# Kernel tuning notes

Measured on AMD Instinct MI355X. Metric: run time of the kernel, lower is better.

Reference implementation:

```python
import jax, jax.numpy as jnp
import numpy as np

EPS = 1e-5

def _ln(x, g, b):
    m = jnp.mean(x, axis=-1, keepdims=True)
    v = jnp.var(x, axis=-1, keepdims=True)
    return (x - m) / jnp.sqrt(v + EPS) * g + b

def setup_inputs() -> dict:
    key = jax.random.key(0)
    ks = jax.random.split(key, 16)
    B, N, CZ, C = 1, 512, 128, 16
    s_cz = 1.0 / np.sqrt(CZ)
    s_c = 1.0 / np.sqrt(C)
    def lin(k, fan_in, shape):
        return jax.random.uniform(k, shape, jnp.float32, -1.0, 1.0) / np.sqrt(fan_in)
    return {
        'x': jax.random.normal(ks[0], (B, N, N, CZ), jnp.float32),
        'Wa1': lin(ks[1], CZ, (CZ, C)), 'ba1': lin(ks[2], CZ, (C,)),
        'Wa2': lin(ks[3], CZ, (CZ, C)), 'ba2': lin(ks[4], CZ, (C,)),
        'Wb1': lin(ks[5], CZ, (CZ, C)), 'bb1': lin(ks[6], CZ, (C,)),
        'Wb2': lin(ks[7], CZ, (CZ, C)), 'bb2': lin(ks[8], CZ, (C,)),
        'ln2_g': jnp.ones((C,), jnp.float32), 'ln2_b': jnp.zeros((C,), jnp.float32),
        'Wg': lin(ks[9], CZ, (CZ, CZ)), 'bg': lin(ks[10], CZ, (CZ,)),
        'Wz': lin(ks[11], C, (C, CZ)), 'bz': lin(ks[12], C, (CZ,)),
    }

def reference(x, Wa1, ba1, Wa2, ba2, Wb1, bb1, Wb2, bb2, ln2_g, ln2_b, Wg, bg, Wz, bz):
    # NOTE: original code computes z=ln1(x) then overwrites z=x, so ln1 is a no-op.
    direction = 'outgoing'
    a = jax.nn.sigmoid((x @ Wa1 + ba1) * (x @ Wa2 + ba2))  # [B,N,N,c]
    b = jax.nn.sigmoid((x @ Wb1 + bb1) * (x @ Wb2 + bb2))  # [B,N,N,c]
    if direction == 'incoming':
        a = jnp.swapaxes(a, 1, 2)
        b = jnp.swapaxes(b, 1, 2)
    g = jax.nn.sigmoid(x @ Wg + bg)  # [B,N,N,c_z]
    # z[b,i,j,c] = sum_k a[b,i,k,c] * b[b,k,j,c]  (per-channel triangle matmul)
    z = jnp.einsum('bikc,bkjc->bijc', a, b)
    return g * (_ln(z, ln2_g, ln2_b) @ Wz + bz)
```

## Files before the change

### kernel.cpp

```cpp
#include <hip/hip_runtime.h>


#define NN 512
#define PP (NN*NN)
#define CZD 128
#define CD 16
#define LN_EPS 1e-5f

typedef unsigned short u16;
typedef __bf16 bf16x8 __attribute__((ext_vector_type(8)));
typedef float  f32x4  __attribute__((ext_vector_type(4)));

#define OFF_A  0u
#define OFF_B  8388608u
#define OFF_Z  16777216u
#define OFF_G  33554432u
#define OFF_WT 100663296u
#define OFF_BC 100712448u

__device__ __forceinline__ float bf2f(u16 u) {
    union { unsigned int i; float f; } v; v.i = ((unsigned int)u) << 16; return v.f;
}
__device__ __forceinline__ u16 f2bf(float f) {
    union { __bf16 b; u16 u; } v; v.b = (__bf16)f; return v.u;
}
__device__ __forceinline__ float sigmoidf(float x) { return 1.0f / (1.0f + __expf(-x)); }

__device__ __forceinline__ int swz(int row, int bytecol) {
    return row * 256 + ((((bytecol >> 4) + row) & 15) << 4) + (bytecol & 15);
}

__global__ void pack_w(const float* __restrict__ Wa1, const float* __restrict__ Wa2,
                       const float* __restrict__ Wb1, const float* __restrict__ Wb2,
                       const float* __restrict__ Wg,
                       const float* __restrict__ ba1, const float* __restrict__ ba2,
                       const float* __restrict__ bb1, const float* __restrict__ bb2,
                       const float* __restrict__ bg,
                       u16* __restrict__ wt, float* __restrict__ bc) {
    int idx = blockIdx.x * 256 + threadIdx.x;
    int n = idx >> 7, k = idx & 127;
    float v;
    if      (n < 16) v = Wa1[k * CD + n];
    else if (n < 32) v = Wa2[k * CD + (n - 16)];
    else if (n < 48) v = Wb1[k * CD + (n - 32)];
    else if (n < 64) v = Wb2[k * CD + (n - 48)];
    else             v = Wg [k * CZD + (n - 64)];
    wt[n * CZD + k] = f2bf(v);
    if (idx < 192) {
        float b;
        if      (idx < 16) b = ba1[idx];
        else if (idx < 32) b = ba2[idx - 16];
        else if (idx < 48) b = bb1[idx - 32];
        else if (idx < 64) b = bb2[idx - 48];
        else               b = bg [idx - 64];
        bc[idx] = b;
    }
}

__global__ __launch_bounds__(512, 4) void proj_kernel(const float* __restrict__ x,
                                                      const u16* __restrict__ wt,
                                                      const float* __restrict__ bc,
                                                      u16* __restrict__ a_ws, u16* __restrict__ b_ws,
                                                      u16* __restrict__ g_ws) {
    __shared__ __align__(16) char lds[49152];
    char* Wl = lds;
    char* aT = lds;
    char* bT = lds + 4096;
    char* gT = lds + 8192;
    const int t = threadIdx.x;
    const int wv = t >> 6, lane = t & 63, l16 = lane & 15, quad = lane >> 4;
    const long pos0 = (long)blockIdx.x * 128;

    const float* xrow = x + (pos0 + wv * 16 + l16) * CZD + quad * 8;
    float4 xa[4][2];
#pragma unroll
    for (int ks = 0; ks < 4; ++ks) {
        xa[ks][0] = *reinterpret_cast<const float4*>(xrow + ks * 32);
        xa[ks][1] = *reinterpret_cast<const float4*>(xrow + ks * 32 + 4);
    }

#pragma unroll
    for (int i = 0; i < 6; ++i) {
        int c = t + 512 * i;
        int n = c >> 4, g = c & 15;
        uint4 v = *reinterpret_cast<const uint4*>(wt + n * CZD + g * 8);
        *reinterpret_cast<uint4*>(Wl + swz(n, g * 16)) = v;
    }

    bf16x8 af[4];
#pragma unroll
    for (int ks = 0; ks < 4; ++ks) {
        union { u16 s[8]; bf16x8 v; } tb;
        tb.s[0] = f2bf(xa[ks][0].x); tb.s[1] = f2bf(xa[ks][0].y);
        tb.s[2] = f2bf(xa[ks][0].z); tb.s[3] = f2bf(xa[ks][0].w);
        tb.s[4] = f2bf(xa[ks][1].x); tb.s[5] = f2bf(xa[ks][1].y);
        tb.s[6] = f2bf(xa[ks][1].z); tb.s[7] = f2bf(xa[ks][1].w);
        af[ks] = tb.v;
    }
    __syncthreads();

    f32x4 acc[12];
#pragma unroll
    for (int ct = 0; ct < 12; ++ct) acc[ct] = (f32x4){0.f, 0.f, 0.f, 0.f};
#pragma unroll
    for (int ks = 0; ks < 4; ++ks)
#pragma unroll
        for (int ct = 0; ct < 12; ++ct) {
            bf16x8 wb = *reinterpret_cast<const bf16x8*>(Wl + swz(ct * 16 + l16, ks * 64 + quad * 16));
            acc[ct] = __builtin_amdgcn_mfma_f32_16x16x32_bf16(af[ks], wb, acc[ct], 0, 0, 0);
        }
    __syncthreads();

    {
        const float ba1 = bc[l16], ba2 = bc[16 + l16], bb1 = bc[32 + l16], bb2 = bc[48 + l16];
        u16 av[4], bv[4];
#pragma unroll
        for (int r = 0; r < 4; ++r) {
            av[r] = f2bf(sigmoidf((acc[0][r] + ba1) * (acc[1][r] + ba2)));
            bv[r] = f2bf(sigmoidf((acc[2][r] + bb1) * (acc[3][r] + bb2)));
        }
        *reinterpret_cast<uint2*>(aT + swz(l16, wv * 32 + quad * 8)) = *reinterpret_cast<const uint2*>(av);
        *reinterpret_cast<uint2*>(bT + swz(l16, wv * 32 + quad * 8)) = *reinterpret_cast<const uint2*>(bv);
#pragma unroll
        for (int ct = 0; ct < 8; ++ct) {
            const float bgv = bc[64 + ct * 16 + l16];
#pragma unroll
            for (int r = 0; r < 4; ++r) {
                int pos = wv * 16 + quad * 4 + r;
                *reinterpret_cast<u16*>(gT + swz(pos, ct * 32 + l16 * 2)) =
                    f2bf(sigmoidf(acc[4 + ct][r] + bgv));
            }
        }
    }
    __syncthreads();

    if (t < 256) {
        int ch = t >> 4, i = t & 15;
        uint4 v = *reinterpret_cast<const uint4*>(aT + swz(ch, i * 16));
        *reinterpret_cast<uint4*>(a_ws + (long)ch * PP + pos0 + i * 8) = v;
    } else {
        int u = t - 256;
        int ch = u >> 4, i = u & 15;
        uint4 v = *reinterpret_cast<const uint4*>(bT + swz(ch, i * 16));
        *reinterpret_cast<uint4*>(b_ws + (long)ch * PP + pos0 + i * 8) = v;
    }
#pragma unroll
    for (int i = 0; i < 4; ++i) {
        int c = t + 512 * i;
        int pos = c >> 4, g = c & 15;
        uint4 v = *reinterpret_cast<const uint4*>(gT + swz(pos, g * 16));
        *reinterpret_cast<uint4*>(g_ws + (pos0 + pos) * CZD + g * 8) = v;
    }
}

__global__ __launch_bounds__(512) void tri_kernel(const u16* __restrict__ a_ws,
                                                  const u16* __restrict__ b_ws,
                                                  float* __restrict__ z_ws) {
    __shared__ __align__(16) char Alds[16384];
    __shared__ __align__(16) char Btl [16384];
    __shared__ __align__(16) char Brow[16384];
    const int t = threadIdx.x;
    const int wv = t >> 6, lane = t & 63, l16 = lane & 15, quad = lane >> 4;
    const int wr = wv >> 2, wc = wv & 3;
    const int c = blockIdx.y;
    const int i0 = (blockIdx.x >> 2) * 128, j0 = (blockIdx.x & 3) * 128;
    const u16* Ap = a_ws + (long)c * PP;
    const u16* Bp = b_ws + (long)c * PP;

    f32x4 acc[4][2];
#pragma unroll
    for (int m = 0; m < 4; ++m)
#pragma unroll
        for (int n = 0; n < 2; ++n) acc[m][n] = (f32x4){0.f, 0.f, 0.f, 0.f};

    for (int k0 = 0; k0 < NN; k0 += 64) {
#pragma unroll
        for (int i = 0; i < 2; ++i) {
            int ch = t + 512 * i;
            int r = ch >> 3, ko = (ch & 7) * 8;
            uint4 v = *reinterpret_cast<const uint4*>(Ap + (long)(i0 + r) * NN + k0 + ko);
            *reinterpret_cast<uint4*>(Alds + r * 128 + ((ko * 2) ^ ((r & 7) << 4))) = v;
        }
#pragma unroll
        for (int i = 0; i < 2; ++i) {
            int ch = t + 512 * i;
            int k = ch >> 4, jo = (ch & 15) * 8;
            uint4 v = *reinterpret_cast<const uint4*>(Bp + (long)(k0 + k) * NN + j0 + jo);
            *reinterpret_cast<uint4*>(Brow + k * 256 + jo * 2) = v;
        }
        __syncthreads();
#pragma unroll
        for (int i = 0; i < 2; ++i) {
            int ch = t + 512 * i;
            int j = ch & 127, kg = ch >> 7;
            union { u16 s[8]; uint4 v; } tb;
#pragma unroll
            for (int m = 0; m < 8; ++m)
                tb.s[m] = *reinterpret_cast<const u16*>(Brow + (kg * 8 + m) * 256 + j * 2);
            *reinterpret_cast<uint4*>(Btl + j * 128 + ((kg ^ (j & 7)) << 4)) = tb.v;
        }
        __syncthreads();
#pragma unroll
        for (int ks = 0; ks < 2; ++ks) {
            bf16x8 af[4];
#pragma unroll
            for (int m = 0; m < 4; ++m) {
                int row = wr * 64 + m * 16 + l16;
                af[m] = *reinterpret_cast<const bf16x8*>(
                    Alds + row * 128 + ((ks * 64 + quad * 16) ^ ((row & 7) << 4)));
            }
#pragma unroll
            for (int n = 0; n < 2; ++n) {
                int jrow = wc * 32 + n * 16 + l16;
                bf16x8 bf = *reinterpret_cast<const bf16x8*>(
                    Btl + jrow * 128 + (((ks * 4 + quad) ^ (jrow & 7)) << 4));
#pragma unroll
                for (int m = 0; m < 4; ++m)
                    acc[m][n] = __builtin_amdgcn_mfma_f32_16x16x32_bf16(af[m], bf, acc[m][n], 0, 0, 0);
            }
        }
        __syncthreads();
    }
    float* Zp = z_ws + (long)c * PP;
#pragma unroll
    for (int m = 0; m < 4; ++m)
#pragma unroll
        for (int n = 0; n < 2; ++n)
#pragma unroll
            for (int r = 0; r < 4; ++r)
                Zp[(long)(i0 + wr * 64 + m * 16 + quad * 4 + r) * NN + j0 + wc * 32 + n * 16 + l16]
                    = acc[m][n][r];
}

__global__ __launch_bounds__(512) void out_kernel(const float* __restrict__ z_ws,
                                                  const u16* __restrict__ g_ws,
                                                  const float* __restrict__ Wz, const float* __restrict__ bz,
                                                  const float* __restrict__ lng, const float* __restrict__ lnb,
                                                  float* __restrict__ out) {
    __shared__ __align__(16) float zt[16][128];
    __shared__ __align__(16) float nl[128][20];
    __shared__ __align__(16) float wzs[16][128];
    __shared__ float bzl[128];
    __shared__ float lg[16], lb[16];
    const int t = threadIdx.x;
    const long pos0 = (long)blockIdx.x * 128;

    {
        int ch = t >> 5, off = (t & 31) * 4;
        const float4 v = *reinterpret_cast<const float4*>(z_ws + (long)ch * PP + pos0 + off);
        *reinterpret_cast<float4*>(&zt[ch][off]) = v;
    }
    {
        int idx = t * 4;
        const float4 v = *reinterpret_cast<const float4*>(Wz + idx);
        *reinterpret_cast<float4*>(&wzs[idx >> 7][idx & 127]) = v;
    }
    if (t < 128)      bzl[t] = bz[t];
    else if (t < 144) lg[t - 128] = lng[t - 128];
    else if (t < 160) lb[t - 144] = lnb[t - 144];
    __syncthreads();

    {
        int p = t & 127, cgr = t >> 7;
        float m = 0.f;
#pragma unroll
        for (int c0 = 0; c0 < 16; ++c0) m += zt[c0][p];
        m *= (1.f / 16.f);
        float v = 0.f;
#pragma unroll
        for (int c0 = 0; c0 < 16; ++c0) { float d = zt[c0][p] - m; v += d * d; }
        v *= (1.f / 16.f);
        float s = rsqrtf(v + LN_EPS);
#pragma unroll
        for (int cc = 0; cc < 4; ++cc) {
            int c0 = cgr * 4 + cc;
            nl[p][c0] = (zt[c0][p] - m) * s * lg[c0] + lb[c0];
        }
    }
    __syncthreads();

    const int czp = (t & 63) * 2, pg = t >> 6;
    float wzr[32];
#pragma unroll
    for (int c0 = 0; c0 < 16; ++c0) {
        wzr[2 * c0]     = wzs[c0][czp];
        wzr[2 * c0 + 1] = wzs[c0][czp + 1];
    }
    const float bz0 = bzl[czp], bz1 = bzl[czp + 1];
    const unsigned int* gp = reinterpret_cast<const unsigned int*>(g_ws);
#pragma unroll
    for (int pp2 = 0; pp2 < 16; ++pp2) {
        int p = pg * 16 + pp2;
        const float4* np = reinterpret_cast<const float4*>(&nl[p][0]);
        float y0 = bz0, y1 = bz1;
#pragma unroll
        for (int c4 = 0; c4 < 4; ++c4) {
            float4 nv = np[c4];
            y0 += nv.x * wzr[(c4 * 4 + 0) * 2] + nv.y * wzr[(c4 * 4 + 1) * 2] +
                  nv.z * wzr[(c4 * 4 + 2) * 2] + nv.w * wzr[(c4 * 4 + 3) * 2];
            y1 += nv.x * wzr[(c4 * 4 + 0) * 2 + 1] + nv.y * wzr[(c4 * 4 + 1) * 2 + 1] +
                  nv.z * wzr[(c4 * 4 + 2) * 2 + 1] + nv.w * wzr[(c4 * 4 + 3) * 2 + 1];
        }
        long o = (pos0 + p) * CZD + czp;
        unsigned int gg = gp[o >> 1];
        float g0 = bf2f((u16)(gg & 0xffffu));
        float g1 = bf2f((u16)(gg >> 16));
        float2 res; res.x = g0 * y0; res.y = g1 * y1;
        *reinterpret_cast<float2*>(out + o) = res;
    }
}

extern "C" void kernel_launch(void* const* d_in, const int* in_sizes, int n_in,
                              void* d_out, int out_size, void* d_ws, size_t ws_size,
                              hipStream_t stream) {
    const float* x   = (const float*)d_in[0];
    const float* Wa1 = (const float*)d_in[1];
    const float* ba1 = (const float*)d_in[2];
    const float* Wa2 = (const float*)d_in[3];
    const float* ba2 = (const float*)d_in[4];
    const float* Wb1 = (const float*)d_in[5];
    const float* bb1 = (const float*)d_in[6];
    const float* Wb2 = (const float*)d_in[7];
    const float* bb2 = (const float*)d_in[8];
    const float* lng = (const float*)d_in[9];
    const float* lnb = (const float*)d_in[10];
    const float* Wg  = (const float*)d_in[11];
    const float* bg  = (const float*)d_in[12];
    const float* Wz  = (const float*)d_in[13];
    const float* bz  = (const float*)d_in[14];
    float* out = (float*)d_out;
    char* ws = (char*)d_ws;
    u16*   a_ws = (u16*)(ws + OFF_A);
    u16*   b_ws = (u16*)(ws + OFF_B);
    float* z_ws = (float*)(ws + OFF_Z);
    u16*   g_ws = (u16*)(ws + OFF_G);
    u16*   wt   = (u16*)(ws + OFF_WT);
    float* bc   = (float*)(ws + OFF_BC);

    hipLaunchKernelGGL(pack_w, dim3(96), dim3(256), 0, stream,
                       Wa1, Wa2, Wb1, Wb2, Wg, ba1, ba2, bb1, bb2, bg, wt, bc);
    hipLaunchKernelGGL(proj_kernel, dim3(2048), dim3(512), 0, stream, x, wt, bc, a_ws, b_ws, g_ws);
    hipLaunchKernelGGL(tri_kernel, dim3(16, 16), dim3(512), 0, stream, a_ws, b_ws, z_ws);
    hipLaunchKernelGGL(out_kernel, dim3(2048), dim3(512), 0, stream, z_ws, g_ws, Wz, bz, lng, lnb, out);
}
```

Before: 318.2 us.

## Transpose B directly into LDS and double-tile the output kernel with z prefetch

```diff
diff --git a/kernel.cpp b/kernel.cpp
--- a/kernel.cpp
+++ b/kernel.cpp
@@ -158,7 +158,6 @@
                                                   float* __restrict__ z_ws) {
     __shared__ __align__(16) char Alds[16384];
     __shared__ __align__(16) char Btl [16384];
-    __shared__ __align__(16) char Brow[16384];
     const int t = threadIdx.x;
     const int wv = t >> 6, lane = t & 63, l16 = lane & 15, quad = lane >> 4;
     const int wr = wv >> 2, wc = wv & 3;
@@ -183,21 +182,17 @@
         }
 #pragma unroll
         for (int i = 0; i < 2; ++i) {
-            int ch = t + 512 * i;
-            int k = ch >> 4, jo = (ch & 15) * 8;
-            uint4 v = *reinterpret_cast<const uint4*>(Bp + (long)(k0 + k) * NN + j0 + jo);
-            *reinterpret_cast<uint4*>(Brow + k * 256 + jo * 2) = v;
-        }
-        __syncthreads();
-#pragma unroll
-        for (int i = 0; i < 2; ++i) {
-            int ch = t + 512 * i;
-            int j = ch & 127, kg = ch >> 7;
-            union { u16 s[8]; uint4 v; } tb;
-#pragma unroll
-            for (int m = 0; m < 8; ++m)
-                tb.s[m] = *reinterpret_cast<const u16*>(Brow + (kg * 8 + m) * 256 + j * 2);
-            *reinterpret_cast<uint4*>(Btl + j * 128 + ((kg ^ (j & 7)) << 4)) = tb.v;
+            int chk = t + 512 * i;
+            int k = chk >> 4, jo = (chk & 15) * 8;
+            union { uint4 v; u16 s[8]; } tb;
+            tb.v = *reinterpret_cast<const uint4*>(Bp + (long)(k0 + k) * NN + j0 + jo);
+            const int kg = k >> 3, kl = (k & 7) * 2;
+#pragma unroll
+            for (int jj = 0; jj < 8; ++jj) {
+                int j = jo + jj;
+                int gran = ((kg ^ (j & 7)) + (j >> 3)) & 7;
+                *reinterpret_cast<u16*>(Btl + j * 128 + gran * 16 + kl) = tb.s[jj];
+            }
         }
         __syncthreads();
 #pragma unroll
@@ -212,8 +207,8 @@
 #pragma unroll
             for (int n = 0; n < 2; ++n) {
                 int jrow = wc * 32 + n * 16 + l16;
-                bf16x8 bf = *reinterpret_cast<const bf16x8*>(
-                    Btl + jrow * 128 + (((ks * 4 + quad) ^ (jrow & 7)) << 4));
+                int gran = (((ks * 4 + quad) ^ (jrow & 7)) + (jrow >> 3)) & 7;
+                bf16x8 bf = *reinterpret_cast<const bf16x8*>(Btl + jrow * 128 + gran * 16);
 #pragma unroll
                 for (int m = 0; m < 4; ++m)
                     acc[m][n] = __builtin_amdgcn_mfma_f32_16x16x32_bf16(af[m], bf, acc[m][n], 0, 0, 0);
@@ -243,13 +238,13 @@
     __shared__ float bzl[128];
     __shared__ float lg[16], lb[16];
     const int t = threadIdx.x;
-    const long pos0 = (long)blockIdx.x * 128;
-
-    {
-        int ch = t >> 5, off = (t & 31) * 4;
-        const float4 v = *reinterpret_cast<const float4*>(z_ws + (long)ch * PP + pos0 + off);
-        *reinterpret_cast<float4*>(&zt[ch][off]) = v;
-    }
+    const long tbase = (long)blockIdx.x * 256;
+
+    const int zch = t >> 5, zoff = (t & 31) * 4;
+    const float* zp = z_ws + (long)zch * PP + tbase + zoff;
+    const float4 zv0 = *reinterpret_cast<const float4*>(zp);
+    const float4 zv1 = *reinterpret_cast<const float4*>(zp + 128);
+
     {
         int idx = t * 4;
         const float4 v = *reinterpret_cast<const float4*>(Wz + idx);
@@ -258,25 +253,7 @@
     if (t < 128)      bzl[t] = bz[t];
     else if (t < 144) lg[t - 128] = lng[t - 128];
     else if (t < 160) lb[t - 144] = lnb[t - 144];
-    __syncthreads();
-
-    {
-        int p = t & 127, cgr = t >> 7;
-        float m = 0.f;
-#pragma unroll
-        for (int c0 = 0; c0 < 16; ++c0) m += zt[c0][p];
-        m *= (1.f / 16.f);
-        float v = 0.f;
-#pragma unroll
-        for (int c0 = 0; c0 < 16; ++c0) { float d = zt[c0][p] - m; v += d * d; }
-        v *= (1.f / 16.f);
-        float s = rsqrtf(v + LN_EPS);
-#pragma unroll
-        for (int cc = 0; cc < 4; ++cc) {
-            int c0 = cgr * 4 + cc;
-            nl[p][c0] = (zt[c0][p] - m) * s * lg[c0] + lb[c0];
-        }
-    }
+    *reinterpret_cast<float4*>(&zt[zch][zoff]) = zv0;
     __syncthreads();
 
     const int czp = (t & 63) * 2, pg = t >> 6;
@@ -288,25 +265,52 @@
     }
     const float bz0 = bzl[czp], bz1 = bzl[czp + 1];
     const unsigned int* gp = reinterpret_cast<const unsigned int*>(g_ws);
-#pragma unroll
-    for (int pp2 = 0; pp2 < 16; ++pp2) {
-        int p = pg * 16 + pp2;
-        const float4* np = reinterpret_cast<const float4*>(&nl[p][0]);
-        float y0 = bz0, y1 = bz1;
-#pragma unroll
-        for (int c4 = 0; c4 < 4; ++c4) {
-            float4 nv = np[c4];
-            y0 += nv.x * wzr[(c4 * 4 + 0) * 2] + nv.y * wzr[(c4 * 4 + 1) * 2] +
-                  nv.z * wzr[(c4 * 4 + 2) * 2] + nv.w * wzr[(c4 * 4 + 3) * 2];
-            y1 += nv.x * wzr[(c4 * 4 + 0) * 2 + 1] + nv.y * wzr[(c4 * 4 + 1) * 2 + 1] +
-                  nv.z * wzr[(c4 * 4 + 2) * 2 + 1] + nv.w * wzr[(c4 * 4 + 3) * 2 + 1];
-        }
-        long o = (pos0 + p) * CZD + czp;
-        unsigned int gg = gp[o >> 1];
-        float g0 = bf2f((u16)(gg & 0xffffu));
-        float g1 = bf2f((u16)(gg >> 16));
-        float2 res; res.x = g0 * y0; res.y = g1 * y1;
-        *reinterpret_cast<float2*>(out + o) = res;
+
+#pragma unroll
+    for (int it = 0; it < 2; ++it) {
+        const long pos0 = tbase + it * 128;
+        {
+            int p = t & 127, cgr = t >> 7;
+            float m = 0.f;
+#pragma unroll
+            for (int c0 = 0; c0 < 16; ++c0) m += zt[c0][p];
+            m *= (1.f / 16.f);
+            float v = 0.f;
+#pragma unroll
+            for (int c0 = 0; c0 < 16; ++c0) { float d = zt[c0][p] - m; v += d * d; }
+            v *= (1.f / 16.f);
+            float s = rsqrtf(v + LN_EPS);
+#pragma unroll
+            for (int cc = 0; cc < 4; ++cc) {
+                int c0 = cgr * 4 + cc;
+                nl[p][c0] = (zt[c0][p] - m) * s * lg[c0] + lb[c0];
+            }
+        }
+        __syncthreads();
+        if (it == 0)
+            *reinterpret_cast<float4*>(&zt[zch][zoff]) = zv1;
+
+#pragma unroll
+        for (int pp2 = 0; pp2 < 16; ++pp2) {
+            int p = pg * 16 + pp2;
+            const float4* np = reinterpret_cast<const float4*>(&nl[p][0]);
+            float y0 = bz0, y1 = bz1;
+#pragma unroll
+            for (int c4 = 0; c4 < 4; ++c4) {
+                float4 nv = np[c4];
+                y0 += nv.x * wzr[(c4 * 4 + 0) * 2] + nv.y * wzr[(c4 * 4 + 1) * 2] +
+                      nv.z * wzr[(c4 * 4 + 2) * 2] + nv.w * wzr[(c4 * 4 + 3) * 2];
+                y1 += nv.x * wzr[(c4 * 4 + 0) * 2 + 1] + nv.y * wzr[(c4 * 4 + 1) * 2 + 1] +
+                      nv.z * wzr[(c4 * 4 + 2) * 2 + 1] + nv.w * wzr[(c4 * 4 + 3) * 2 + 1];
+            }
+            long o = (pos0 + p) * CZD + czp;
+            unsigned int gg = gp[o >> 1];
+            float g0 = bf2f((u16)(gg & 0xffffu));
+            float g1 = bf2f((u16)(gg >> 16));
+            float2 res; res.x = g0 * y0; res.y = g1 * y1;
+            *reinterpret_cast<float2*>(out + o) = res;
+        }
+        __syncthreads();
     }
 }
 
@@ -341,5 +345,5 @@
                        Wa1, Wa2, Wb1, Wb2, Wg, ba1, ba2, bb1, bb2, bg, wt, bc);
     hipLaunchKernelGGL(proj_kernel, dim3(2048), dim3(512), 0, stream, x, wt, bc, a_ws, b_ws, g_ws);
     hipLaunchKernelGGL(tri_kernel, dim3(16, 16), dim3(512), 0, stream, a_ws, b_ws, z_ws);
-    hipLaunchKernelGGL(out_kernel, dim3(2048), dim3(512), 0, stream, z_ws, g_ws, Wz, bz, lng, lnb, out);
-}
+    hipLaunchKernelGGL(out_kernel, dim3(1024), dim3(512), 0, stream, z_ws, g_ws, Wz, bz, lng, lnb, out);
+}
```

After: 310.2 us. 1.03x faster.
